# Optimization experiments

Measured on AMD Instinct MI355X. Metric: run time of the kernel, lower is better.

## Reference

```python
import jax, jax.numpy as jnp
import numpy as np

N = 40000
E = 640000
D_IN = 128
D_H = 128
D_OUT = 1


def setup_inputs() -> dict:
    key = jax.random.key(0)
    ks = jax.random.split(key, 10)
    s = 1.0 / np.sqrt(D_IN)
    sh = 1.0 / np.sqrt(D_H)
    return {
        "x": jax.random.normal(ks[0], (N, D_IN), dtype=jnp.float32),
        "edge_index": jax.random.randint(ks[1], (2, E), 0, N, dtype=jnp.int64),
        # conv1: lin_l (neighbors, has bias), lin_r (root, no bias)
        "W1l": jax.random.uniform(ks[2], (D_IN, D_H), jnp.float32, -s, s),
        "b1": jnp.zeros((D_H,), jnp.float32),
        "W1r": jax.random.uniform(ks[3], (D_IN, D_H), jnp.float32, -s, s),
        # conv2
        "W2l": jax.random.uniform(ks[4], (D_H, D_H), jnp.float32, -sh, sh),
        "b2": jnp.zeros((D_H,), jnp.float32),
        "W2r": jax.random.uniform(ks[5], (D_H, D_H), jnp.float32, -sh, sh),
        # final linear
        "Wo": jax.random.uniform(ks[6], (D_H, D_OUT), jnp.float32, -sh, sh),
        "bo": jnp.zeros((D_OUT,), jnp.float32),
    }


def _mean_aggregate(x, src, dst, num_nodes):
    # mean over incoming edges per target node (PyG SAGEConv default aggr='mean')
    msg_sum = jax.ops.segment_sum(x[src], dst, num_segments=num_nodes)  # [N, D]
    deg = jax.ops.segment_sum(jnp.ones((src.shape[0],), x.dtype), dst,
                              num_segments=num_nodes)
    return msg_sum / jnp.maximum(deg, 1.0)[:, None]


def _sage_conv(x, src, dst, Wl, b, Wr):
    # out = lin_l(mean_agg(neighbors)) + lin_r(x)
    agg = _mean_aggregate(x, src, dst, x.shape[0])
    return agg @ Wl + b + x @ Wr


def reference(x, edge_index, W1l, b1, W1r, W2l, b2, W2r, Wo, bo):
    src, dst = edge_index[0], edge_index[1]
    h = jax.nn.relu(_sage_conv(x, src, dst, W1l, b1, W1r))
    h = jax.nn.relu(_sage_conv(h, src, dst, W2l, b2, W2r))
    return h @ Wo + bo
```

## Files before the change

kernel.cpp:

```cpp
#include <hip/hip_runtime.h>
#include <hip/hip_bf16.h>


#define DH 128

typedef __attribute__((ext_vector_type(8))) short bf16x8;
typedef __attribute__((ext_vector_type(4))) float f32x4;

__device__ __forceinline__ unsigned short f2bf_rne(float f) {
    unsigned int u = __float_as_uint(f);
    return (unsigned short)((u + 0x7FFFu + ((u >> 16) & 1u)) >> 16);
}
__device__ __forceinline__ float bf2f(unsigned short h) {
    return __uint_as_float(((unsigned int)h) << 16);
}


__global__ void deg_kernel(const int* __restrict__ dst, int* __restrict__ deg, int E) {
    int i = blockIdx.x * blockDim.x + threadIdx.x;
    if (i < E) atomicAdd(&deg[dst[i]], 1);
}

__global__ __launch_bounds__(256) void scan1_kernel(
    const int* __restrict__ deg, int* __restrict__ offs, int* __restrict__ bsum, int N)
{
    __shared__ int tmp[256];
    int tid = threadIdx.x;
    int i = blockIdx.x * 256 + tid;
    int v = (i < N) ? deg[i] : 0;
    tmp[tid] = v;
    __syncthreads();
    #pragma unroll
    for (int off = 1; off < 256; off <<= 1) {
        int t = (tid >= off) ? tmp[tid - off] : 0;
        __syncthreads();
        tmp[tid] += t;
        __syncthreads();
    }
    if (i < N) offs[i] = tmp[tid] - v;
    if (tid == 255) bsum[blockIdx.x] = tmp[255];
}

__global__ __launch_bounds__(256) void scan2_kernel(
    const int* __restrict__ bsum, int* __restrict__ boffs, int nb)
{
    __shared__ int tmp[256];
    int tid = threadIdx.x;
    int v = (tid < nb) ? bsum[tid] : 0;
    tmp[tid] = v;
    __syncthreads();
    #pragma unroll
    for (int off = 1; off < 256; off <<= 1) {
        int t = (tid >= off) ? tmp[tid - off] : 0;
        __syncthreads();
        tmp[tid] += t;
        __syncthreads();
    }
    if (tid < nb) boffs[tid] = tmp[tid] - v;
}

__global__ void fill_kernel(const int* __restrict__ src, const int* __restrict__ dst,
                            const int* __restrict__ offs, const int* __restrict__ boffs,
                            int* __restrict__ cursor, int* __restrict__ csr, int E)
{
    int e = blockIdx.x * blockDim.x + threadIdx.x;
    if (e >= E) return;
    int d = dst[e];
    int pos = atomicAdd(&cursor[d], 1);
    csr[offs[d] + boffs[d >> 8] + pos] = src[e];
}


__device__ __forceinline__ void f4add(float4& a, const float4 b) {
    a.x += b.x; a.y += b.y; a.z += b.z; a.w += b.w;
}

__global__ __launch_bounds__(256) void gather_mean_kernel(
    const float* __restrict__ feat, const int* __restrict__ csr,
    const int* __restrict__ offs, const int* __restrict__ boffs,
    const int* __restrict__ deg, float* __restrict__ out, int N)
{
    int node = blockIdx.x * 4 + (threadIdx.x >> 6);
    if (node >= N) return;
    int lane = threadIdx.x & 63;
    int c = lane & 31;
    int half = lane >> 5;

    int start = offs[node] + boffs[node >> 8];
    int dg = deg[node];
    int end = start + dg;

    float4 a0 = make_float4(0.f, 0.f, 0.f, 0.f);
    float4 a1 = make_float4(0.f, 0.f, 0.f, 0.f);
    int e = start + half;
    for (; e + 2 < end; e += 4) {
        int s0 = csr[e];
        int s1 = csr[e + 2];
        f4add(a0, *(const float4*)&feat[(size_t)s0 * DH + c * 4]);
        f4add(a1, *(const float4*)&feat[(size_t)s1 * DH + c * 4]);
    }
    if (e < end) f4add(a0, *(const float4*)&feat[(size_t)csr[e] * DH + c * 4]);
    f4add(a0, a1);
    a0.x += __shfl_down(a0.x, 32);
    a0.y += __shfl_down(a0.y, 32);
    a0.z += __shfl_down(a0.z, 32);
    a0.w += __shfl_down(a0.w, 32);
    if (half == 0) {
        float sc = 1.0f / (float)max(dg, 1);
        a0.x *= sc; a0.y *= sc; a0.z *= sc; a0.w *= sc;
        *(float4*)&out[(size_t)node * DH + c * 4] = a0;
    }
}


__global__ __launch_bounds__(256) void wprep_kernel(
    const float* __restrict__ W1l, const float* __restrict__ W1r,
    const float* __restrict__ W2l, const float* __restrict__ W2r,
    unsigned short* __restrict__ whi, unsigned short* __restrict__ wlo)
{
    int tid = blockIdx.x * 256 + threadIdx.x;
    if (tid >= 2 * 8 * 8 * 64) return;
    int lane = tid & 63;
    int f = (tid >> 6) & 7;
    int t = (tid >> 9) & 7;
    int conv = tid >> 12;
    const float* Wl = conv ? W2l : W1l;
    const float* Wr = conv ? W2r : W1r;
    int c = f * 16 + (lane & 15);
    int kb = t * 32 + (lane >> 4) * 8;
    size_t off = (size_t)tid * 8;
    #pragma unroll
    for (int j = 0; j < 8; ++j) {
        int k = kb + j;
        float w = (k < 128) ? Wl[k * 128 + c] : Wr[(k - 128) * 128 + c];
        unsigned short h = f2bf_rne(w);
        whi[off + j] = h;
        wlo[off + j] = f2bf_rne(w - bf2f(h));
    }
}


__global__ __launch_bounds__(256) void sage_mfma_kernel(
    const float* __restrict__ Agg, const float* __restrict__ X,
    const unsigned short* __restrict__ whi, const unsigned short* __restrict__ wlo,
    const float* __restrict__ bias, float* __restrict__ H)
{
    const int l = threadIdx.x & 63;
    const int wv = threadIdx.x >> 6;
    const int row0 = blockIdx.x * 64 + wv * 16;
    const int r = l & 15;
    const int kq = l >> 4;

    f32x4 acc[8];
    #pragma unroll
    for (int f = 0; f < 8; ++f) {
        float b = bias[f * 16 + r];
        acc[f] = (f32x4){b, b, b, b};
    }

    #pragma unroll
    for (int t = 0; t < 8; ++t) {
        const float* A = (t < 4) ? Agg : X;
        const float* ap = &A[(size_t)(row0 + r) * DH + (t & 3) * 32 + kq * 8];
        float4 f0 = *(const float4*)ap;
        float4 f1 = *(const float4*)(ap + 4);
        float a[8] = {f0.x, f0.y, f0.z, f0.w, f1.x, f1.y, f1.z, f1.w};
        bf16x8 ahi, alo;
        #pragma unroll
        for (int j = 0; j < 8; ++j) {
            unsigned short h = f2bf_rne(a[j]);
            ahi[j] = (short)h;
            alo[j] = (short)f2bf_rne(a[j] - bf2f(h));
        }
        const unsigned short* bh = whi + ((size_t)(t * 8) * 64 + l) * 8;
        const unsigned short* bl = wlo + ((size_t)(t * 8) * 64 + l) * 8;
        #pragma unroll
        for (int f = 0; f < 8; ++f) {
            bf16x8 bhi = *(const bf16x8*)(bh + (size_t)f * 64 * 8);
            bf16x8 blo = *(const bf16x8*)(bl + (size_t)f * 64 * 8);
            acc[f] = __builtin_amdgcn_mfma_f32_16x16x32_bf16(ahi, bhi, acc[f], 0, 0, 0);
            acc[f] = __builtin_amdgcn_mfma_f32_16x16x32_bf16(alo, bhi, acc[f], 0, 0, 0);
            acc[f] = __builtin_amdgcn_mfma_f32_16x16x32_bf16(ahi, blo, acc[f], 0, 0, 0);
        }
    }

    #pragma unroll
    for (int f = 0; f < 8; ++f) {
        int col = f * 16 + r;
        #pragma unroll
        for (int q = 0; q < 4; ++q) {
            int row = row0 + kq * 4 + q;
            H[(size_t)row * DH + col] = fmaxf(acc[f][q], 0.0f);
        }
    }
}

__global__ __launch_bounds__(256) void out_kernel(
    const float* __restrict__ H, const float* __restrict__ Wo,
    const float* __restrict__ bo, float* __restrict__ out, int N)
{
    int row = blockIdx.x * 4 + (threadIdx.x >> 6);
    int lane = threadIdx.x & 63;
    if (row >= N) return;
    float2 h = *(const float2*)&H[(size_t)row * DH + lane * 2];
    float2 w = *(const float2*)&Wo[lane * 2];
    float v = h.x * w.x + h.y * w.y;
    #pragma unroll
    for (int off = 32; off; off >>= 1) v += __shfl_down(v, off);
    if (lane == 0) out[row] = v + bo[0];
}

extern "C" void kernel_launch(void* const* d_in, const int* in_sizes, int n_in,
                              void* d_out, int out_size, void* d_ws, size_t ws_size,
                              hipStream_t stream) {
    const float* x   = (const float*)d_in[0];
    const int*   ei  = (const int*)d_in[1];
    const float* W1l = (const float*)d_in[2];
    const float* b1  = (const float*)d_in[3];
    const float* W1r = (const float*)d_in[4];
    const float* W2l = (const float*)d_in[5];
    const float* b2  = (const float*)d_in[6];
    const float* W2r = (const float*)d_in[7];
    const float* Wo  = (const float*)d_in[8];
    const float* bo  = (const float*)d_in[9];
    float* out = (float*)d_out;

    const int N = in_sizes[0] / DH;
    const int E = in_sizes[1] / 2;
    const int* src = ei;
    const int* dst = ei + E;
    const int nb = (N + 255) / 256;

    float* A = (float*)d_ws;
    float* B = A + (size_t)N * DH;
    int* deg    = (int*)(B + (size_t)N * DH);
    int* offs   = deg + N;
    int* cursor = offs + N;
    int* bsum   = cursor + N;
    int* boffs  = bsum + 256;
    int* csr    = boffs + 256;
    unsigned short* whi = (unsigned short*)(csr + E);
    unsigned short* wlo = whi + 2 * 32768;

    hipMemsetAsync(deg, 0, (size_t)N * sizeof(int), stream);
    hipMemsetAsync(cursor, 0, (size_t)N * sizeof(int), stream);
    deg_kernel<<<(E + 255) / 256, 256, 0, stream>>>(dst, deg, E);
    wprep_kernel<<<32, 256, 0, stream>>>(W1l, W1r, W2l, W2r, whi, wlo);
    scan1_kernel<<<nb, 256, 0, stream>>>(deg, offs, bsum, N);
    scan2_kernel<<<1, 256, 0, stream>>>(bsum, boffs, nb);
    fill_kernel<<<(E + 255) / 256, 256, 0, stream>>>(src, dst, offs, boffs, cursor, csr, E);

    gather_mean_kernel<<<(N + 3) / 4, 256, 0, stream>>>(x, csr, offs, boffs, deg, A, N);
    sage_mfma_kernel<<<N / 64, 256, 0, stream>>>(A, x, whi, wlo, b1, B);

    gather_mean_kernel<<<(N + 3) / 4, 256, 0, stream>>>(B, csr, offs, boffs, deg, A, N);
    sage_mfma_kernel<<<N / 64, 256, 0, stream>>>(A, B, whi + 32768, wlo + 32768, b2, A);

    out_kernel<<<(N + 3) / 4, 256, 0, stream>>>(A, Wo, bo, out, N);
}
```

Before: 288.3 us.

## Fuse mean aggregation into SAGE MFMA kernel with bf16 gather and output head

Merges the neighbour-mean gather into the per-tile MFMA kernel, staging the aggregated rows in swizzled LDS instead of writing and re-reading an fp32 intermediate. Neighbour features are gathered from a bf16 copy (a new conversion kernel for x, and a bf16 shadow of h1), which halves gather bytes. The final linear head is folded into the second conv's epilogue, removing the separate output kernel. Risks include lower occupancy from 32KB LDS, serial per-wave gather of 16 rows, and a bf16 rounding error on aggregated features.

```diff
diff --git a/kernel.cpp b/kernel.cpp
--- a/kernel.cpp
+++ b/kernel.cpp
@@ -13,6 +13,12 @@
 }
 __device__ __forceinline__ float bf2f(unsigned short h) {
     return __uint_as_float(((unsigned int)h) << 16);
+}
+__device__ __forceinline__ float bflo(unsigned int u) {
+    return __uint_as_float(u << 16);
+}
+__device__ __forceinline__ float bfhi(unsigned int u) {
+    return __uint_as_float(u & 0xffff0000u);
 }
 
 
@@ -71,45 +77,16 @@
 }
 
 
-__device__ __forceinline__ void f4add(float4& a, const float4 b) {
-    a.x += b.x; a.y += b.y; a.z += b.z; a.w += b.w;
-}
-
-__global__ __launch_bounds__(256) void gather_mean_kernel(
-    const float* __restrict__ feat, const int* __restrict__ csr,
-    const int* __restrict__ offs, const int* __restrict__ boffs,
-    const int* __restrict__ deg, float* __restrict__ out, int N)
-{
-    int node = blockIdx.x * 4 + (threadIdx.x >> 6);
-    if (node >= N) return;
-    int lane = threadIdx.x & 63;
-    int c = lane & 31;
-    int half = lane >> 5;
-
-    int start = offs[node] + boffs[node >> 8];
-    int dg = deg[node];
-    int end = start + dg;
-
-    float4 a0 = make_float4(0.f, 0.f, 0.f, 0.f);
-    float4 a1 = make_float4(0.f, 0.f, 0.f, 0.f);
-    int e = start + half;
-    for (; e + 2 < end; e += 4) {
-        int s0 = csr[e];
-        int s1 = csr[e + 2];
-        f4add(a0, *(const float4*)&feat[(size_t)s0 * DH + c * 4]);
-        f4add(a1, *(const float4*)&feat[(size_t)s1 * DH + c * 4]);
-    }
-    if (e < end) f4add(a0, *(const float4*)&feat[(size_t)csr[e] * DH + c * 4]);
-    f4add(a0, a1);
-    a0.x += __shfl_down(a0.x, 32);
-    a0.y += __shfl_down(a0.y, 32);
-    a0.z += __shfl_down(a0.z, 32);
-    a0.w += __shfl_down(a0.w, 32);
-    if (half == 0) {
-        float sc = 1.0f / (float)max(dg, 1);
-        a0.x *= sc; a0.y *= sc; a0.z *= sc; a0.w *= sc;
-        *(float4*)&out[(size_t)node * DH + c * 4] = a0;
-    }
+__global__ __launch_bounds__(256) void tobf_kernel(
+    const float* __restrict__ in, unsigned short* __restrict__ out, int n4)
+{
+    int i = blockIdx.x * 256 + threadIdx.x;
+    if (i >= n4) return;
+    float4 v = ((const float4*)in)[i];
+    ushort4 o;
+    o.x = f2bf_rne(v.x); o.y = f2bf_rne(v.y);
+    o.z = f2bf_rne(v.z); o.w = f2bf_rne(v.w);
+    ((ushort4*)out)[i] = o;
 }
 
 
@@ -140,14 +117,60 @@
 }
 
 
-__global__ __launch_bounds__(256) void sage_mfma_kernel(
-    const float* __restrict__ Agg, const float* __restrict__ X,
+template<int HEAD>
+__global__ __launch_bounds__(256) void sage_fused_kernel(
+    const unsigned short* __restrict__ featbf, const float* __restrict__ Xself,
+    const int* __restrict__ csr, const int* __restrict__ offs,
+    const int* __restrict__ boffs, const int* __restrict__ deg,
     const unsigned short* __restrict__ whi, const unsigned short* __restrict__ wlo,
-    const float* __restrict__ bias, float* __restrict__ H)
-{
+    const float* __restrict__ bias,
+    float* __restrict__ Hf, unsigned short* __restrict__ Hbf,
+    const float* __restrict__ Wo, const float* __restrict__ bo,
+    float* __restrict__ outp)
+{
+    __shared__ float4 lds4[64 * 32];
     const int l = threadIdx.x & 63;
     const int wv = threadIdx.x >> 6;
-    const int row0 = blockIdx.x * 64 + wv * 16;
+    const int wrow0 = blockIdx.x * 64 + wv * 16;
+
+    {
+        const int half = l >> 5;
+        const int c = l & 31;
+        for (int rr = 0; rr < 16; ++rr) {
+            int node = wrow0 + rr;
+            int dg = deg[node];
+            int start = offs[node] + boffs[node >> 8];
+            int end = start + dg;
+            float4 a0 = make_float4(0.f, 0.f, 0.f, 0.f);
+            float4 a1 = make_float4(0.f, 0.f, 0.f, 0.f);
+            int e = start + half;
+            for (; e + 2 < end; e += 4) {
+                int s0 = csr[e], s1 = csr[e + 2];
+                uint2 v0 = *(const uint2*)&featbf[(size_t)s0 * DH + c * 4];
+                uint2 v1 = *(const uint2*)&featbf[(size_t)s1 * DH + c * 4];
+                a0.x += bflo(v0.x); a0.y += bfhi(v0.x);
+                a0.z += bflo(v0.y); a0.w += bfhi(v0.y);
+                a1.x += bflo(v1.x); a1.y += bfhi(v1.x);
+                a1.z += bflo(v1.y); a1.w += bfhi(v1.y);
+            }
+            if (e < end) {
+                uint2 v0 = *(const uint2*)&featbf[(size_t)csr[e] * DH + c * 4];
+                a0.x += bflo(v0.x); a0.y += bfhi(v0.x);
+                a0.z += bflo(v0.y); a0.w += bfhi(v0.y);
+            }
+            a0.x += a1.x; a0.y += a1.y; a0.z += a1.z; a0.w += a1.w;
+            a0.x += __shfl_down(a0.x, 32);
+            a0.y += __shfl_down(a0.y, 32);
+            a0.z += __shfl_down(a0.z, 32);
+            a0.w += __shfl_down(a0.w, 32);
+            if (half == 0) {
+                float sc = 1.0f / (float)max(dg, 1);
+                a0.x *= sc; a0.y *= sc; a0.z *= sc; a0.w *= sc;
+                lds4[(wv * 16 + rr) * 32 + (c ^ (rr & 7))] = a0;
+            }
+        }
+    }
+
     const int r = l & 15;
     const int kq = l >> 4;
 
@@ -160,11 +183,20 @@
 
     #pragma unroll
     for (int t = 0; t < 8; ++t) {
-        const float* A = (t < 4) ? Agg : X;
-        const float* ap = &A[(size_t)(row0 + r) * DH + (t & 3) * 32 + kq * 8];
-        float4 f0 = *(const float4*)ap;
-        float4 f1 = *(const float4*)(ap + 4);
-        float a[8] = {f0.x, f0.y, f0.z, f0.w, f1.x, f1.y, f1.z, f1.w};
+        float a[8];
+        if (t < 4) {
+            int fb = t * 8 + kq * 2;
+            float4 f0 = lds4[(wv * 16 + r) * 32 + (fb ^ (r & 7))];
+            float4 f1 = lds4[(wv * 16 + r) * 32 + ((fb + 1) ^ (r & 7))];
+            a[0] = f0.x; a[1] = f0.y; a[2] = f0.z; a[3] = f0.w;
+            a[4] = f1.x; a[5] = f1.y; a[6] = f1.z; a[7] = f1.w;
+        } else {
+            const float* ap = &Xself[(size_t)(wrow0 + r) * DH + (t & 3) * 32 + kq * 8];
+            float4 f0 = *(const float4*)ap;
+            float4 f1 = *(const float4*)(ap + 4);
+            a[0] = f0.x; a[1] = f0.y; a[2] = f0.z; a[3] = f0.w;
+            a[4] = f1.x; a[5] = f1.y; a[6] = f1.z; a[7] = f1.w;
+        }
         bf16x8 ahi, alo;
         #pragma unroll
         for (int j = 0; j < 8; ++j) {
@@ -184,30 +216,37 @@
         }
     }
 
-    #pragma unroll
-    for (int f = 0; f < 8; ++f) {
-        int col = f * 16 + r;
-        #pragma unroll
-        for (int q = 0; q < 4; ++q) {
-            int row = row0 + kq * 4 + q;
-            H[(size_t)row * DH + col] = fmaxf(acc[f][q], 0.0f);
-        }
-    }
-}
-
-__global__ __launch_bounds__(256) void out_kernel(
-    const float* __restrict__ H, const float* __restrict__ Wo,
-    const float* __restrict__ bo, float* __restrict__ out, int N)
-{
-    int row = blockIdx.x * 4 + (threadIdx.x >> 6);
-    int lane = threadIdx.x & 63;
-    if (row >= N) return;
-    float2 h = *(const float2*)&H[(size_t)row * DH + lane * 2];
-    float2 w = *(const float2*)&Wo[lane * 2];
-    float v = h.x * w.x + h.y * w.y;
-    #pragma unroll
-    for (int off = 32; off; off >>= 1) v += __shfl_down(v, off);
-    if (lane == 0) out[row] = v + bo[0];
+    if (HEAD == 0) {
+        #pragma unroll
+        for (int f = 0; f < 8; ++f) {
+            int col = f * 16 + r;
+            #pragma unroll
+            for (int q = 0; q < 4; ++q) {
+                int row = wrow0 + kq * 4 + q;
+                float v = fmaxf(acc[f][q], 0.0f);
+                Hf[(size_t)row * DH + col] = v;
+                Hbf[(size_t)row * DH + col] = f2bf_rne(v);
+            }
+        }
+    } else {
+        float wo[8];
+        #pragma unroll
+        for (int f = 0; f < 8; ++f) wo[f] = Wo[f * 16 + r];
+        float s[4] = {0.f, 0.f, 0.f, 0.f};
+        #pragma unroll
+        for (int f = 0; f < 8; ++f)
+            #pragma unroll
+            for (int q = 0; q < 4; ++q)
+                s[q] += fmaxf(acc[f][q], 0.0f) * wo[f];
+        #pragma unroll
+        for (int m = 1; m < 16; m <<= 1) {
+            s[0] += __shfl_xor(s[0], m);
+            s[1] += __shfl_xor(s[1], m);
+            s[2] += __shfl_xor(s[2], m);
+            s[3] += __shfl_xor(s[3], m);
+        }
+        if (r < 4) outp[wrow0 + kq * 4 + r] = s[r] + bo[0];
+    }
 }
 
 extern "C" void kernel_launch(void* const* d_in, const int* in_sizes, int n_in,
@@ -231,9 +270,10 @@
     const int* dst = ei + E;
     const int nb = (N + 255) / 256;
 
-    float* A = (float*)d_ws;
-    float* B = A + (size_t)N * DH;
-    int* deg    = (int*)(B + (size_t)N * DH);
+    float* h1 = (float*)d_ws;
+    unsigned short* xbf  = (unsigned short*)(h1 + (size_t)N * DH);
+    unsigned short* h1bf = xbf + (size_t)N * DH;
+    int* deg    = (int*)(h1bf + (size_t)N * DH);
     int* offs   = deg + N;
     int* cursor = offs + N;
     int* bsum   = cursor + N;
@@ -245,16 +285,17 @@
     hipMemsetAsync(deg, 0, (size_t)N * sizeof(int), stream);
     hipMemsetAsync(cursor, 0, (size_t)N * sizeof(int), stream);
     deg_kernel<<<(E + 255) / 256, 256, 0, stream>>>(dst, deg, E);
+    tobf_kernel<<<(N * DH / 4 + 255) / 256, 256, 0, stream>>>(x, xbf, N * DH / 4);
     wprep_kernel<<<32, 256, 0, stream>>>(W1l, W1r, W2l, W2r, whi, wlo);
     scan1_kernel<<<nb, 256, 0, stream>>>(deg, offs, bsum, N);
     scan2_kernel<<<1, 256, 0, stream>>>(bsum, boffs, nb);
     fill_kernel<<<(E + 255) / 256, 256, 0, stream>>>(src, dst, offs, boffs, cursor, csr, E);
 
-    gather_mean_kernel<<<(N + 3) / 4, 256, 0, stream>>>(x, csr, offs, boffs, deg, A, N);
-    sage_mfma_kernel<<<N / 64, 256, 0, stream>>>(A, x, whi, wlo, b1, B);
-
-    gather_mean_kernel<<<(N + 3) / 4, 256, 0, stream>>>(B, csr, offs, boffs, deg, A, N);
-    sage_mfma_kernel<<<N / 64, 256, 0, stream>>>(A, B, whi + 32768, wlo + 32768, b2, A);
-
-    out_kernel<<<(N + 3) / 4, 256, 0, stream>>>(A, Wo, bo, out, N);
-}
+    sage_fused_kernel<0><<<N / 64, 256, 0, stream>>>(
+        xbf, x, csr, offs, boffs, deg, whi, wlo, b1, h1, h1bf,
+        nullptr, nullptr, nullptr);
+
+    sage_fused_kernel<1><<<N / 64, 256, 0, stream>>>(
+        h1bf, h1, csr, offs, boffs, deg, whi + 32768, wlo + 32768, b2,
+        nullptr, nullptr, Wo, bo, out);
+}
```

Result: slower. 310.6 us (+7.7%).
